# Optimization experiments

Measured on AMD Instinct MI355X. Metric: run time of the kernel, lower is better.

The kernel has to match this reference:

```python
import jax, jax.numpy as jnp
import numpy as np

B, N, DIN, H, DOUT = 32, 1024, 256, 256, 256
NEG = 9000000000000000.0  # -9e15 masking trick from the original code


def setup_inputs() -> dict:
    key = jax.random.key(0)
    ks = jax.random.split(key, 10)
    x = jax.random.normal(ks[0], (B, N, DIN), dtype=jnp.float32)
    # binary float mask (1 = edge present)
    mask = jax.random.randint(ks[1], (B, N, N), 0, 2).astype(jnp.float32)
    s = 0.02
    Wv = jax.random.normal(ks[2], (DIN, H), dtype=jnp.float32) * s
    bv = jnp.zeros((H,), jnp.float32)
    Wk = jax.random.normal(ks[3], (DIN, H), dtype=jnp.float32) * s
    bk = jnp.zeros((H,), jnp.float32)
    Wq = jax.random.normal(ks[4], (DIN, H), dtype=jnp.float32) * s
    bq = jnp.zeros((H,), jnp.float32)
    Wo = jax.random.normal(ks[5], (H, DOUT), dtype=jnp.float32) * s
    bo = jnp.zeros((DOUT,), jnp.float32)
    return {"x": x, "mask": mask, "Wv": Wv, "bv": bv, "Wk": Wk, "bk": bk,
            "Wq": Wq, "bq": bq, "Wo": Wo, "bo": bo}


def reference(x, mask, Wv, bv, Wk, bk, Wq, bq, Wo, bo):
    # x: [B,N,din], mask: [B,N,N]
    v = jax.nn.relu(x @ Wv + bv)              # [B,N,H]
    q = jax.nn.relu(x @ Wq + bq)              # [B,N,H]
    k = jax.nn.relu(x @ Wk + bk)              # [B,N,H]
    scores = jnp.einsum('bnh,bmh->bnm', q, k)  # QK^T, [B,N,N]
    att = jax.nn.softmax(scores * mask - NEG * (1.0 - mask), axis=-1)
    out = jnp.einsum('bnm,bmh->bnh', att, v)   # AV
    return jax.nn.relu(out @ Wo + bo)          # [B,N,d_out]
```

## Files before the change

kernel.cpp:

```cpp
#include <hip/hip_runtime.h>


typedef __attribute__((ext_vector_type(4))) float    f32x4;
typedef __attribute__((ext_vector_type(8))) short    s16x8;
typedef __attribute__((ext_vector_type(4))) short    s16x4;
typedef __attribute__((ext_vector_type(4))) unsigned u32x4;

__device__ __forceinline__ short f2b(float f) {
    union { float f; unsigned u; } v; v.f = f;
    unsigned r = v.u + 0x7FFFu + ((v.u >> 16) & 1u);
    return (short)(r >> 16);
}

__device__ __forceinline__ void gl_lds16(const short* g, short* l) {
    __builtin_amdgcn_global_load_lds(
        (const __attribute__((address_space(1))) unsigned int*)g,
        (__attribute__((address_space(3))) unsigned int*)l, 16, 0, 0);
}

__global__ void prep_w(const float* __restrict__ Wq, const float* __restrict__ Wk,
                       const float* __restrict__ Wv, const float* __restrict__ Wo,
                       short* __restrict__ Wt) {
    int idx = blockIdx.x * 256 + threadIdx.x;
    int w = idx >> 16, rem = idx & 65535;
    int n = rem >> 8, kk = rem & 255;
    const float* W = (w == 0) ? Wq : (w == 1) ? Wk : (w == 2) ? Wv : Wo;
    Wt[idx] = f2b(W[kk * 256 + n]);
}

__global__ __launch_bounds__(256) void qkv_gemm(
        const float* __restrict__ x, const short* __restrict__ Wt,
        const float* __restrict__ bq, const float* __restrict__ bk, const float* __restrict__ bv,
        const float* __restrict__ mask, unsigned* __restrict__ mp,
        short* __restrict__ qO, short* __restrict__ kO, short* __restrict__ vtO) {
    __shared__ short a_lds[128][72];
    __shared__ short b_lds[3][64][72];
    const int tid = threadIdx.x;
    const int bm = blockIdx.x >> 2, bn = blockIdx.x & 3;
    const int s0 = bm * 128, n0 = bn * 64;
    const int wid = tid >> 6, l = tid & 63, lo4 = l & 15, hi4 = l >> 4;
    const int wm = wid >> 1, wn = wid & 1;

    {
        int gid = blockIdx.x * 256 + tid;
        const float* p = mask + (size_t)gid * 128;
        u32x4 ob;
        #pragma unroll
        for (int wgi = 0; wgi < 4; ++wgi) {
            unsigned bb = 0;
            #pragma unroll
            for (int i = 0; i < 8; ++i) {
                f32x4 v = *(const f32x4*)(p + wgi * 32 + i * 4);
                bb |= (unsigned)(v.x != 0.f) << (i * 4);
                bb |= (unsigned)(v.y != 0.f) << (i * 4 + 1);
                bb |= (unsigned)(v.z != 0.f) << (i * 4 + 2);
                bb |= (unsigned)(v.w != 0.f) << (i * 4 + 3);
            }
            ob[wgi] = bb;
        }
        *(u32x4*)(mp + (size_t)gid * 4) = ob;
    }

    f32x4 acc[3][4][2];
    #pragma unroll
    for (int w = 0; w < 3; ++w)
        #pragma unroll
        for (int mi = 0; mi < 4; ++mi)
            #pragma unroll
            for (int ni = 0; ni < 2; ++ni)
                acc[w][mi][ni] = (f32x4){0.f, 0.f, 0.f, 0.f};

    for (int kt = 0; kt < 4; ++kt) {
        const int k0 = kt * 64;
        #pragma unroll
        for (int i = 0; i < 8; ++i) {
            int ch = i * 256 + tid;
            int row = ch >> 4, c4 = (ch & 15) * 4;
            f32x4 xv = *(const f32x4*)(x + (size_t)(s0 + row) * 256 + k0 + c4);
            s16x4 pk = { f2b(xv.x), f2b(xv.y), f2b(xv.z), f2b(xv.w) };
            *(s16x4*)&a_lds[row][c4] = pk;
        }
        #pragma unroll
        for (int w = 0; w < 3; ++w) {
            #pragma unroll
            for (int i = 0; i < 2; ++i) {
                int ch = i * 256 + tid;
                int n = ch >> 3, c8 = (ch & 7) * 8;
                *(s16x8*)&b_lds[w][n][c8] =
                    *(const s16x8*)(Wt + (size_t)w * 65536 + (size_t)(n0 + n) * 256 + k0 + c8);
            }
        }
        __syncthreads();
        s16x8 af[4][2];
        #pragma unroll
        for (int mi = 0; mi < 4; ++mi)
            #pragma unroll
            for (int kk = 0; kk < 2; ++kk)
                af[mi][kk] = *(s16x8*)&a_lds[wm * 64 + mi * 16 + lo4][kk * 32 + hi4 * 8];
        #pragma unroll
        for (int w = 0; w < 3; ++w)
            #pragma unroll
            for (int ni = 0; ni < 2; ++ni)
                #pragma unroll
                for (int kk = 0; kk < 2; ++kk) {
                    s16x8 bfr = *(s16x8*)&b_lds[w][wn * 32 + ni * 16 + lo4][kk * 32 + hi4 * 8];
                    #pragma unroll
                    for (int mi = 0; mi < 4; ++mi)
                        acc[w][mi][ni] = __builtin_amdgcn_mfma_f32_16x16x32_bf16(
                            af[mi][kk], bfr, acc[w][mi][ni], 0, 0, 0);
                }
        __syncthreads();
    }

    const float* bias[3] = { bq, bk, bv };
    for (int w = 0; w < 3; ++w) {
        #pragma unroll
        for (int mi = 0; mi < 4; ++mi)
            #pragma unroll
            for (int ni = 0; ni < 2; ++ni)
                #pragma unroll
                for (int j = 0; j < 4; ++j) {
                    int r = wm * 64 + mi * 16 + hi4 * 4 + j;
                    int c = wn * 32 + ni * 16 + lo4;
                    float v = acc[w][mi][ni][j] + bias[w][n0 + c];
                    a_lds[r][c] = f2b(fmaxf(v, 0.f));
                }
        __syncthreads();
        if (w == 0) {
            #pragma unroll
            for (int i = 0; i < 4; ++i) {
                int ch = i * 256 + tid;
                int row = ch >> 3, c8 = (ch & 7) * 8;
                *(s16x8*)(qO + (size_t)(s0 + row) * 256 + n0 + c8) = *(s16x8*)&a_lds[row][c8];
            }
        } else if (w == 1) {
            #pragma unroll
            for (int i = 0; i < 4; ++i) {
                int ch = i * 256 + tid;
                int row = ch >> 3, c8 = (ch & 7) * 8;
                int swz = ((c8 >> 3) ^ (row & 7)) * 8;
                *(s16x8*)(kO + (size_t)(s0 + row) * 256 + n0 + swz) = *(s16x8*)&a_lds[row][c8];
            }
        } else {
            int bb = s0 >> 10, nn = s0 & 1023;
            #pragma unroll
            for (int i = 0; i < 4; ++i) {
                int ch = i * 256 + tid;
                int h = ch >> 4, sc = (ch & 15) * 8;
                s16x8 t;
                #pragma unroll
                for (int e = 0; e < 8; ++e) t[e] = a_lds[sc + e][h];
                int cil = sc >> 3;
                int swz = (cil & 8) | ((cil & 7) ^ ((n0 + h) & 7));
                *(s16x8*)(vtO + ((size_t)bb * 256 + n0 + h) * 1024 + nn + swz * 8) = t;
            }
        }
        __syncthreads();
    }
}

__global__ __launch_bounds__(512) void attn(
        const short* __restrict__ q, const short* __restrict__ k,
        const short* __restrict__ vt, const unsigned* __restrict__ mp,
        short* __restrict__ attv) {
    __shared__ short kbuf[2][16384];
    __shared__ short vbuf[2][16384];
    __shared__ short p_lds[8][16][72];
    const int tid = threadIdx.x, wid = tid >> 6, l = tid & 63;
    const int lo4 = l & 15, hi4 = l >> 4;
    const int bid = blockIdx.x;
    const int swz = (bid & 7) * 32 + (bid >> 3);
    const int b = swz >> 3, qb = swz & 7;
    const int q0 = qb * 128 + wid * 16;
    const size_t bq_row = (size_t)b * 1024 + q0;

    const short* kb  = k  + (size_t)b * 1024 * 256;
    const short* vtg = vt + (size_t)b * 256 * 1024;
    const unsigned* mpb = mp + ((size_t)b << 15);

#define STAGE_K(bufi, c0_) do { const short* sg_ = kb + (size_t)(c0_) * 256;          \
    _Pragma("unroll") for (int i_ = 0; i_ < 4; ++i_) { int cb_ = i_ * 512 + wid * 64; \
        gl_lds16(sg_ + (size_t)(cb_ + l) * 8, &kbuf[bufi][cb_ * 8]); } } while (0)
#define STAGE_V(bufi, c0_) do {                                                       \
    _Pragma("unroll") for (int i_ = 0; i_ < 4; ++i_) { int cb_ = i_ * 512 + wid * 64; \
        int ch_ = cb_ + l; int h_ = ch_ >> 3, cc_ = ch_ & 7;                          \
        gl_lds16(vtg + (size_t)h_ * 1024 + (c0_) + cc_ * 8, &vbuf[bufi][cb_ * 8]); } } while (0)
#define LOAD_MASK(dst, c0_) do {                                                      \
    _Pragma("unroll") for (int j_ = 0; j_ < 4; ++j_) {                                \
        size_t wi_ = (size_t)(q0 + hi4 * 4 + j_) * 32 + ((c0_) >> 5);                 \
        dst[j_ * 2] = mpb[wi_]; dst[j_ * 2 + 1] = mpb[wi_ + 1]; } } while (0)

    s16x8 qf[8];
    {
        const short* qp = q + (bq_row + lo4) * 256 + hi4 * 8;
        #pragma unroll
        for (int t = 0; t < 8; ++t) qf[t] = *(const s16x8*)(qp + t * 32);
    }
    f32x4 oacc[16];
    #pragma unroll
    for (int t = 0; t < 16; ++t) oacc[t] = (f32x4){0.f, 0.f, 0.f, 0.f};
    float m_run[4] = { -1e30f, -1e30f, -1e30f, -1e30f };
    float l_run[4] = { 0.f, 0.f, 0.f, 0.f };
    unsigned mwc[8], mwn[8];

    STAGE_K(0, 0);
    LOAD_MASK(mwc, 0);
    STAGE_V(0, 0);

    for (int t = 0; t < 16; ++t) {
        const int cur = t & 1;
        const int c0 = t * 64;
        if (t < 15) {
            STAGE_K(cur ^ 1, c0 + 64);
            LOAD_MASK(mwn, c0 + 64);
            asm volatile("s_waitcnt vmcnt(24)" ::: "memory");
        } else {
            asm volatile("s_waitcnt vmcnt(12)" ::: "memory");
        }
        __builtin_amdgcn_s_barrier();
        f32x4 s[4];
        #pragma unroll
        for (int ct = 0; ct < 4; ++ct) s[ct] = (f32x4){0.f, 0.f, 0.f, 0.f};
        __builtin_amdgcn_s_setprio(1);
        #pragma unroll
        for (int ct = 0; ct < 4; ++ct) {
            int row = ct * 16 + lo4, rx = row & 7;
            #pragma unroll
            for (int tt = 0; tt < 8; ++tt) {
                int ch = tt * 4 + hi4;
                int sc = (ch & 24) | ((ch & 7) ^ rx);
                s16x8 kf = *(s16x8*)&kbuf[cur][row * 256 + sc * 8];
                s[ct] = __builtin_amdgcn_mfma_f32_16x16x32_bf16(qf[tt], kf, s[ct], 0, 0, 0);
            }
        }
        __builtin_amdgcn_s_setprio(0);
        float sm[4][4];
        #pragma unroll
        for (int j = 0; j < 4; ++j) {
            unsigned w0 = mwc[j * 2], w1 = mwc[j * 2 + 1];
            sm[0][j] = ((w0 >> lo4) & 1)        ? s[0][j] : -1e30f;
            sm[1][j] = ((w0 >> (16 + lo4)) & 1) ? s[1][j] : -1e30f;
            sm[2][j] = ((w1 >> lo4) & 1)        ? s[2][j] : -1e30f;
            sm[3][j] = ((w1 >> (16 + lo4)) & 1) ? s[3][j] : -1e30f;
        }
        float scale[4], p[4][4];
        #pragma unroll
        for (int j = 0; j < 4; ++j) {
            float tmx = fmaxf(fmaxf(sm[0][j], sm[1][j]), fmaxf(sm[2][j], sm[3][j]));
            tmx = fmaxf(tmx, __shfl_xor(tmx, 1));
            tmx = fmaxf(tmx, __shfl_xor(tmx, 2));
            tmx = fmaxf(tmx, __shfl_xor(tmx, 4));
            tmx = fmaxf(tmx, __shfl_xor(tmx, 8));
            float mnew = fmaxf(m_run[j], tmx);
            scale[j] = __expf(m_run[j] - mnew);
            m_run[j] = mnew;
            float su = 0.f;
            #pragma unroll
            for (int ct = 0; ct < 4; ++ct) { p[ct][j] = __expf(sm[ct][j] - mnew); su += p[ct][j]; }
            su += __shfl_xor(su, 1);
            su += __shfl_xor(su, 2);
            su += __shfl_xor(su, 4);
            su += __shfl_xor(su, 8);
            l_run[j] = l_run[j] * scale[j] + su;
        }
        #pragma unroll
        for (int tt = 0; tt < 16; ++tt)
            #pragma unroll
            for (int j = 0; j < 4; ++j) oacc[tt][j] *= scale[j];
        #pragma unroll
        for (int ct = 0; ct < 4; ++ct)
            #pragma unroll
            for (int j = 0; j < 4; ++j)
                p_lds[wid][hi4 * 4 + j][ct * 16 + lo4] = f2b(p[ct][j]);
        asm volatile("s_waitcnt lgkmcnt(0)" ::: "memory");
        __builtin_amdgcn_sched_barrier(0);
        s16x8 pa0 = *(s16x8*)&p_lds[wid][lo4][hi4 * 8];
        s16x8 pa1 = *(s16x8*)&p_lds[wid][lo4][32 + hi4 * 8];
        if (t < 15) {
            STAGE_V(cur ^ 1, c0 + 64);
            asm volatile("s_waitcnt vmcnt(16)" ::: "memory");
        } else {
            asm volatile("s_waitcnt vmcnt(0)" ::: "memory");
        }
        __builtin_amdgcn_s_barrier();
        __builtin_amdgcn_s_setprio(1);
        #pragma unroll
        for (int nt = 0; nt < 16; ++nt) {
            int h = nt * 16 + lo4, hx = h & 7;
            s16x8 vf0 = *(s16x8*)&vbuf[cur][h * 64 + (hi4 ^ hx) * 8];
            s16x8 vf1 = *(s16x8*)&vbuf[cur][h * 64 + ((hi4 + 4) ^ hx) * 8];
            oacc[nt] = __builtin_amdgcn_mfma_f32_16x16x32_bf16(pa0, vf0, oacc[nt], 0, 0, 0);
            oacc[nt] = __builtin_amdgcn_mfma_f32_16x16x32_bf16(pa1, vf1, oacc[nt], 0, 0, 0);
        }
        __builtin_amdgcn_s_setprio(0);
        if (t < 15) {
            #pragma unroll
            for (int i = 0; i < 8; ++i) mwc[i] = mwn[i];
        }
    }
    float inv[4];
    #pragma unroll
    for (int j = 0; j < 4; ++j) inv[j] = 1.f / l_run[j];
    #pragma unroll
    for (int g = 0; g < 4; ++g) {
        asm volatile("s_waitcnt lgkmcnt(0)" ::: "memory");
        #pragma unroll
        for (int ntl = 0; ntl < 4; ++ntl)
            #pragma unroll
            for (int j = 0; j < 4; ++j)
                p_lds[wid][hi4 * 4 + j][ntl * 16 + lo4] = f2b(oacc[g * 4 + ntl][j] * inv[j]);
        asm volatile("s_waitcnt lgkmcnt(0)" ::: "memory");
        __builtin_amdgcn_sched_barrier(0);
        s16x8 r0 = *(s16x8*)&p_lds[wid][lo4][hi4 * 16];
        s16x8 r1 = *(s16x8*)&p_lds[wid][lo4][hi4 * 16 + 8];
        short* op = attv + (bq_row + lo4) * 256 + g * 64 + hi4 * 16;
        *(s16x8*)op = r0;
        *(s16x8*)(op + 8) = r1;
    }
#undef STAGE_K
#undef STAGE_V
#undef LOAD_MASK
}

__global__ __launch_bounds__(256) void out_gemm(
        const short* __restrict__ a, const short* __restrict__ Wto,
        const float* __restrict__ bo, float* __restrict__ out) {
    __shared__ short a_lds[128][72];
    __shared__ short b_lds[64][72];
    __shared__ float bounce[128][68];
    const int tid = threadIdx.x;
    const int bm = blockIdx.x >> 2, bn = blockIdx.x & 3;
    const int s0 = bm * 128, n0 = bn * 64;
    const int wid = tid >> 6, l = tid & 63, lo4 = l & 15, hi4 = l >> 4;
    const int wm = wid >> 1, wn = wid & 1;
    f32x4 acc[4][2];
    #pragma unroll
    for (int mi = 0; mi < 4; ++mi)
        #pragma unroll
        for (int ni = 0; ni < 2; ++ni) acc[mi][ni] = (f32x4){0.f, 0.f, 0.f, 0.f};

    for (int kt = 0; kt < 4; ++kt) {
        const int k0 = kt * 64;
        #pragma unroll
        for (int i = 0; i < 4; ++i) {
            int ch = i * 256 + tid;
            int row = ch >> 3, c8 = (ch & 7) * 8;
            *(s16x8*)&a_lds[row][c8] = *(const s16x8*)(a + (size_t)(s0 + row) * 256 + k0 + c8);
        }
        #pragma unroll
        for (int i = 0; i < 2; ++i) {
            int ch = i * 256 + tid;
            int n = ch >> 3, c8 = (ch & 7) * 8;
            *(s16x8*)&b_lds[n][c8] = *(const s16x8*)(Wto + (size_t)(n0 + n) * 256 + k0 + c8);
        }
        __syncthreads();
        s16x8 af[4][2];
        #pragma unroll
        for (int mi = 0; mi < 4; ++mi)
            #pragma unroll
            for (int kk = 0; kk < 2; ++kk)
                af[mi][kk] = *(s16x8*)&a_lds[wm * 64 + mi * 16 + lo4][kk * 32 + hi4 * 8];
        #pragma unroll
        for (int ni = 0; ni < 2; ++ni)
            #pragma unroll
            for (int kk = 0; kk < 2; ++kk) {
                s16x8 bfr = *(s16x8*)&b_lds[wn * 32 + ni * 16 + lo4][kk * 32 + hi4 * 8];
                #pragma unroll
                for (int mi = 0; mi < 4; ++mi)
                    acc[mi][ni] = __builtin_amdgcn_mfma_f32_16x16x32_bf16(
                        af[mi][kk], bfr, acc[mi][ni], 0, 0, 0);
            }
        __syncthreads();
    }
    #pragma unroll
    for (int mi = 0; mi < 4; ++mi)
        #pragma unroll
        for (int ni = 0; ni < 2; ++ni)
            #pragma unroll
            for (int j = 0; j < 4; ++j) {
                int r = wm * 64 + mi * 16 + hi4 * 4 + j;
                int c = wn * 32 + ni * 16 + lo4;
                bounce[r][c] = fmaxf(acc[mi][ni][j] + bo[n0 + c], 0.f);
            }
    __syncthreads();
    #pragma unroll
    for (int i = 0; i < 8; ++i) {
        int ch = i * 256 + tid;
        int row = ch >> 4, c4 = (ch & 15) * 4;
        *(f32x4*)(out + (size_t)(s0 + row) * 256 + n0 + c4) = *(f32x4*)&bounce[row][c4];
    }
}

extern "C" void kernel_launch(void* const* d_in, const int* in_sizes, int n_in,
                              void* d_out, int out_size, void* d_ws, size_t ws_size,
                              hipStream_t stream) {
    const float* x    = (const float*)d_in[0];
    const float* mask = (const float*)d_in[1];
    const float* Wv   = (const float*)d_in[2];
    const float* bv   = (const float*)d_in[3];
    const float* Wk   = (const float*)d_in[4];
    const float* bk   = (const float*)d_in[5];
    const float* Wq   = (const float*)d_in[6];
    const float* bq   = (const float*)d_in[7];
    const float* Wo   = (const float*)d_in[8];
    const float* bo   = (const float*)d_in[9];
    float* out = (float*)d_out;

    char* ws = (char*)d_ws;
    short*    Wt  = (short*)ws;
    unsigned* mpW = (unsigned*)(ws + (512 << 10));
    short*    qB  = (short*)(ws + (4608 << 10));
    short*    kB  = qB  + (size_t)32768 * 256;
    short*    vtB = kB  + (size_t)32768 * 256;
    short*    avB = vtB + (size_t)32768 * 256;
    (void)in_sizes; (void)n_in; (void)out_size; (void)ws_size;

    prep_w<<<1024, 256, 0, stream>>>(Wq, Wk, Wv, Wo, Wt);
    qkv_gemm<<<1024, 256, 0, stream>>>(x, Wt, bq, bk, bv, mask, mpW, qB, kB, vtB);
    attn<<<256, 512, 0, stream>>>(qB, kB, vtB, mpW, avB);
    out_gemm<<<1024, 256, 0, stream>>>(avB, Wt + 3 * 65536, bo, out);
}
```

Measured before the change: 150.5 us.

## Read float mask directly in attention instead of pre-packing bitmask

Removes the bit-packing pass over the float mask from the QKV GEMM kernel, along with the packed-bitmask workspace. The attention kernel now loads the float mask values for its own tile, four per row per thread, and compares them against zero inline. The goal is to drop the extra write and read of the packed mask and to overlap the large mask read with attention compute. In exchange, attention issues twice as many smaller, strided global loads per tile, and its vmcnt wait thresholds are raised to match.

```diff
diff --git a/kernel.cpp b/kernel.cpp
--- a/kernel.cpp
+++ b/kernel.cpp
@@ -4,7 +4,6 @@
 typedef __attribute__((ext_vector_type(4))) float    f32x4;
 typedef __attribute__((ext_vector_type(8))) short    s16x8;
 typedef __attribute__((ext_vector_type(4))) short    s16x4;
-typedef __attribute__((ext_vector_type(4))) unsigned u32x4;
 
 __device__ __forceinline__ short f2b(float f) {
     union { float f; unsigned u; } v; v.f = f;
@@ -31,7 +30,6 @@
 __global__ __launch_bounds__(256) void qkv_gemm(
         const float* __restrict__ x, const short* __restrict__ Wt,
         const float* __restrict__ bq, const float* __restrict__ bk, const float* __restrict__ bv,
-        const float* __restrict__ mask, unsigned* __restrict__ mp,
         short* __restrict__ qO, short* __restrict__ kO, short* __restrict__ vtO) {
     __shared__ short a_lds[128][72];
     __shared__ short b_lds[3][64][72];
@@ -40,26 +38,6 @@
     const int s0 = bm * 128, n0 = bn * 64;
     const int wid = tid >> 6, l = tid & 63, lo4 = l & 15, hi4 = l >> 4;
     const int wm = wid >> 1, wn = wid & 1;
-
-    {
-        int gid = blockIdx.x * 256 + tid;
-        const float* p = mask + (size_t)gid * 128;
-        u32x4 ob;
-        #pragma unroll
-        for (int wgi = 0; wgi < 4; ++wgi) {
-            unsigned bb = 0;
-            #pragma unroll
-            for (int i = 0; i < 8; ++i) {
-                f32x4 v = *(const f32x4*)(p + wgi * 32 + i * 4);
-                bb |= (unsigned)(v.x != 0.f) << (i * 4);
-                bb |= (unsigned)(v.y != 0.f) << (i * 4 + 1);
-                bb |= (unsigned)(v.z != 0.f) << (i * 4 + 2);
-                bb |= (unsigned)(v.w != 0.f) << (i * 4 + 3);
-            }
-            ob[wgi] = bb;
-        }
-        *(u32x4*)(mp + (size_t)gid * 4) = ob;
-    }
 
     f32x4 acc[3][4][2];
     #pragma unroll
@@ -161,7 +139,7 @@
 
 __global__ __launch_bounds__(512) void attn(
         const short* __restrict__ q, const short* __restrict__ k,
-        const short* __restrict__ vt, const unsigned* __restrict__ mp,
+        const short* __restrict__ vt, const float* __restrict__ mask,
         short* __restrict__ attv) {
     __shared__ short kbuf[2][16384];
     __shared__ short vbuf[2][16384];
@@ -176,7 +154,7 @@
 
     const short* kb  = k  + (size_t)b * 1024 * 256;
     const short* vtg = vt + (size_t)b * 256 * 1024;
-    const unsigned* mpb = mp + ((size_t)b << 15);
+    const float* mb  = mask + ((size_t)b * 1024 + q0 + hi4 * 4) * 1024 + lo4;
 
 #define STAGE_K(bufi, c0_) do { const short* sg_ = kb + (size_t)(c0_) * 256;          \
     _Pragma("unroll") for (int i_ = 0; i_ < 4; ++i_) { int cb_ = i_ * 512 + wid * 64; \
@@ -187,8 +165,8 @@
         gl_lds16(vtg + (size_t)h_ * 1024 + (c0_) + cc_ * 8, &vbuf[bufi][cb_ * 8]); } } while (0)
 #define LOAD_MASK(dst, c0_) do {                                                      \
     _Pragma("unroll") for (int j_ = 0; j_ < 4; ++j_) {                                \
-        size_t wi_ = (size_t)(q0 + hi4 * 4 + j_) * 32 + ((c0_) >> 5);                 \
-        dst[j_ * 2] = mpb[wi_]; dst[j_ * 2 + 1] = mpb[wi_ + 1]; } } while (0)
+        const float* mr_ = mb + (size_t)j_ * 1024 + (c0_);                            \
+        dst[j_] = (f32x4){ mr_[0], mr_[16], mr_[32], mr_[48] }; } } while (0)
 
     s16x8 qf[8];
     {
@@ -201,10 +179,10 @@
     for (int t = 0; t < 16; ++t) oacc[t] = (f32x4){0.f, 0.f, 0.f, 0.f};
     float m_run[4] = { -1e30f, -1e30f, -1e30f, -1e30f };
     float l_run[4] = { 0.f, 0.f, 0.f, 0.f };
-    unsigned mwc[8], mwn[8];
+    f32x4 mkc[4], mkn[4];
 
     STAGE_K(0, 0);
-    LOAD_MASK(mwc, 0);
+    LOAD_MASK(mkc, 0);
     STAGE_V(0, 0);
 
     for (int t = 0; t < 16; ++t) {
@@ -212,10 +190,10 @@
         const int c0 = t * 64;
         if (t < 15) {
             STAGE_K(cur ^ 1, c0 + 64);
-            LOAD_MASK(mwn, c0 + 64);
-            asm volatile("s_waitcnt vmcnt(24)" ::: "memory");
+            LOAD_MASK(mkn, c0 + 64);
+            asm volatile("s_waitcnt vmcnt(40)" ::: "memory");
         } else {
-            asm volatile("s_waitcnt vmcnt(12)" ::: "memory");
+            asm volatile("s_waitcnt vmcnt(20)" ::: "memory");
         }
         __builtin_amdgcn_s_barrier();
         f32x4 s[4];
@@ -237,11 +215,10 @@
         float sm[4][4];
         #pragma unroll
         for (int j = 0; j < 4; ++j) {
-            unsigned w0 = mwc[j * 2], w1 = mwc[j * 2 + 1];
-            sm[0][j] = ((w0 >> lo4) & 1)        ? s[0][j] : -1e30f;
-            sm[1][j] = ((w0 >> (16 + lo4)) & 1) ? s[1][j] : -1e30f;
-            sm[2][j] = ((w1 >> lo4) & 1)        ? s[2][j] : -1e30f;
-            sm[3][j] = ((w1 >> (16 + lo4)) & 1) ? s[3][j] : -1e30f;
+            sm[0][j] = (mkc[j].x != 0.f) ? s[0][j] : -1e30f;
+            sm[1][j] = (mkc[j].y != 0.f) ? s[1][j] : -1e30f;
+            sm[2][j] = (mkc[j].z != 0.f) ? s[2][j] : -1e30f;
+            sm[3][j] = (mkc[j].w != 0.f) ? s[3][j] : -1e30f;
         }
         float scale[4], p[4][4];
         #pragma unroll
@@ -278,7 +255,7 @@
         s16x8 pa1 = *(s16x8*)&p_lds[wid][lo4][32 + hi4 * 8];
         if (t < 15) {
             STAGE_V(cur ^ 1, c0 + 64);
-            asm volatile("s_waitcnt vmcnt(16)" ::: "memory");
+            asm volatile("s_waitcnt vmcnt(24)" ::: "memory");
         } else {
             asm volatile("s_waitcnt vmcnt(0)" ::: "memory");
         }
@@ -295,7 +272,7 @@
         __builtin_amdgcn_s_setprio(0);
         if (t < 15) {
             #pragma unroll
-            for (int i = 0; i < 8; ++i) mwc[i] = mwn[i];
+            for (int i = 0; i < 4; ++i) mkc[i] = mkn[i];
         }
     }
     float inv[4];
@@ -408,15 +385,14 @@
 
     char* ws = (char*)d_ws;
     short*    Wt  = (short*)ws;
-    unsigned* mpW = (unsigned*)(ws + (512 << 10));
-    short*    qB  = (short*)(ws + (4608 << 10));
+    short*    qB  = (short*)(ws + (1 << 20));
     short*    kB  = qB  + (size_t)32768 * 256;
     short*    vtB = kB  + (size_t)32768 * 256;
     short*    avB = vtB + (size_t)32768 * 256;
     (void)in_sizes; (void)n_in; (void)out_size; (void)ws_size;
 
     prep_w<<<1024, 256, 0, stream>>>(Wq, Wk, Wv, Wo, Wt);
-    qkv_gemm<<<1024, 256, 0, stream>>>(x, Wt, bq, bk, bv, mask, mpW, qB, kB, vtB);
-    attn<<<256, 512, 0, stream>>>(qB, kB, vtB, mpW, avB);
+    qkv_gemm<<<1024, 256, 0, stream>>>(x, Wt, bq, bk, bv, qB, kB, vtB);
+    attn<<<256, 512, 0, stream>>>(qB, kB, vtB, mask, avB);
     out_gemm<<<1024, 256, 0, stream>>>(avB, Wt + 3 * 65536, bo, out);
 }
```

Result: faster. 138.5 us (-8.0%).
